# Kernel tuning notes

Hardware: AMD Instinct MI355X
Metric: run time of the kernel (lower is better)

Reference implementation:

```python
import jax, jax.numpy as jnp
import numpy as np

N_TOKENS = 2048
D_IN = 1024
D_HID = 4096
D_OUT = 1024
N_EXPERTS = 8
TOP_K = 2


def setup_inputs() -> dict:
    key = jax.random.key(0)
    ks = jax.random.split(key, 8)
    s_in = 1.0 / np.sqrt(D_IN)
    s_hid = 1.0 / np.sqrt(D_HID)
    return {
        "x": jax.random.normal(ks[0], (N_TOKENS, D_IN), dtype=jnp.float32),
        # Router Linear(D_IN, E)
        "Wr": jax.random.uniform(ks[1], (D_IN, N_EXPERTS), jnp.float32, -s_in, s_in),
        "br": jax.random.uniform(ks[2], (N_EXPERTS,), jnp.float32, -s_in, s_in),
        # Stacked expert MLP weights [E, ...]
        "W1": jax.random.uniform(ks[3], (N_EXPERTS, D_IN, D_HID), jnp.float32, -s_in, s_in),
        "b1": jax.random.uniform(ks[4], (N_EXPERTS, D_HID), jnp.float32, -s_in, s_in),
        "W2": jax.random.uniform(ks[5], (N_EXPERTS, D_HID, D_OUT), jnp.float32, -s_hid, s_hid),
        "b2": jax.random.uniform(ks[6], (N_EXPERTS, D_OUT), jnp.float32, -s_hid, s_hid),
    }


def reference(x, Wr, br, W1, b1, W2, b2):
    # Router: softmax over expert logits, then top-k
    routing = jax.nn.softmax(x @ Wr + br, axis=-1)            # [N, E]
    topk_w, topk_idx = jax.lax.top_k(routing, TOP_K)          # [N, k] each
    # Combine weights per expert: c[n, e] = sum_i topk_w[n, i] * (topk_idx[n, i] == e)
    onehot = jax.nn.one_hot(topk_idx, N_EXPERTS, dtype=x.dtype)  # [N, k, E]
    combine = jnp.einsum('nk,nke->ne', topk_w, onehot)           # [N, E]
    # Run all experts on all tokens (dense equivalent of the dispatch loop);
    # non-selected experts get combine weight 0, so math matches exactly.
    h = jax.nn.relu(jnp.einsum('nd,edh->neh', x, W1) + b1)       # [N, E, H]
    y = jnp.einsum('neh,ehd->ned', h, W2) + b2                   # [N, E, Dout]
    out = jnp.einsum('ne,ned->nd', combine, y)                   # [N, Dout]
    return out
```

## Files before the change

kernel.cpp:

```cpp
#include <hip/hip_runtime.h>
#include <hip/hip_bf16.h>

#define N_TOKENS 2048
#define D_IN 1024
#define D_HID 4096
#define D_OUT 1024
#define NE 8

typedef __attribute__((ext_vector_type(8))) short s16x8;
typedef __attribute__((ext_vector_type(4))) float f32x4;

__device__ inline unsigned short f2bf(float f) {
  union { float f; unsigned u; } v; v.f = f;
  unsigned u = v.u;
  unsigned r = u + 0x7fff + ((u >> 16) & 1);
  return (unsigned short)(r >> 16);
}

#define GLDS16(gp, lp)                                                          \
  __builtin_amdgcn_global_load_lds(                                             \
      (const __attribute__((address_space(1))) unsigned int*)(gp),              \
      (__attribute__((address_space(3))) unsigned int*)(lp), 16, 0, 0)

__global__ __launch_bounds__(256) void router_kernel(
    const float* __restrict__ x, const float* __restrict__ Wr,
    const float* __restrict__ br, int* __restrict__ cnt, int* __restrict__ tids,
    int4* __restrict__ meta, float2* __restrict__ tw) {
  int wid = threadIdx.x >> 6, lane = threadIdx.x & 63;
  int n = blockIdx.x * 4 + wid;
  const float* xr = x + (size_t)n * D_IN;
  float acc[NE];
#pragma unroll
  for (int e = 0; e < NE; e++) acc[e] = 0.f;
  for (int i = lane; i < D_IN; i += 64) {
    float xv = xr[i];
    const float4* wr = (const float4*)(Wr + (size_t)i * NE);
    float4 w0 = wr[0], w1 = wr[1];
    acc[0] += xv * w0.x; acc[1] += xv * w0.y;
    acc[2] += xv * w0.z; acc[3] += xv * w0.w;
    acc[4] += xv * w1.x; acc[5] += xv * w1.y;
    acc[6] += xv * w1.z; acc[7] += xv * w1.w;
  }
#pragma unroll
  for (int e = 0; e < NE; e++) {
#pragma unroll
    for (int s = 32; s; s >>= 1) acc[e] += __shfl_xor(acc[e], s, 64);
  }
  if (lane == 0) {
    float lg[NE], p[NE];
    float m = -1e30f;
#pragma unroll
    for (int e = 0; e < NE; e++) { lg[e] = acc[e] + br[e]; m = fmaxf(m, lg[e]); }
    float s = 0.f;
#pragma unroll
    for (int e = 0; e < NE; e++) { p[e] = expf(lg[e] - m); s += p[e]; }
    float inv = 1.f / s;
    int i0 = 0;
#pragma unroll
    for (int e = 1; e < NE; e++) if (lg[e] > lg[i0]) i0 = e;
    int i1 = (i0 == 0) ? 1 : 0;
#pragma unroll
    for (int e = 0; e < NE; e++) if (e != i0 && lg[e] > lg[i1]) i1 = e;
    int p0 = atomicAdd(&cnt[i0], 1);
    int p1 = atomicAdd(&cnt[i1], 1);
    tids[i0 * N_TOKENS + p0] = n;
    tids[i1 * N_TOKENS + p1] = n;
    meta[n] = make_int4(i0, p0, i1, p1);
    tw[n] = make_float2(p[i0] * inv, p[i1] * inv);
  }
}

__global__ __launch_bounds__(256) void convx_kernel(const float* __restrict__ x,
                                                    short* __restrict__ xb) {
  int i = (blockIdx.x * 256 + threadIdx.x) * 4;
  float4 v = *(const float4*)(x + i);
  short4 o;
  o.x = (short)f2bf(v.x); o.y = (short)f2bf(v.y);
  o.z = (short)f2bf(v.z); o.w = (short)f2bf(v.w);
  *(short4*)(xb + i) = o;
}

__global__ __launch_bounds__(256) void transconv_kernel(
    const float* __restrict__ src, short* __restrict__ dst, int R, int C) {
  __shared__ float tile[64][65];
  size_t eoff = (size_t)blockIdx.z * R * C;
  int r0 = blockIdx.y * 64, c0 = blockIdx.x * 64;
  const float* s = src + eoff + (size_t)r0 * C + c0;
  int t = threadIdx.x;
  int lc4 = (t & 15) * 4;
  int lr16 = t >> 4;
#pragma unroll
  for (int p = 0; p < 4; p++) {
    int r = p * 16 + lr16;
    float4 v = *(const float4*)(s + (size_t)r * C + lc4);
    tile[r][lc4 + 0] = v.x; tile[r][lc4 + 1] = v.y;
    tile[r][lc4 + 2] = v.z; tile[r][lc4 + 3] = v.w;
  }
  __syncthreads();
  short* d = dst + eoff + (size_t)c0 * R + r0;
  int rr4 = (t & 15) * 4;
  int cc = t >> 4;
#pragma unroll
  for (int p = 0; p < 4; p++) {
    int c = p * 16 + cc;
    short4 o;
    o.x = (short)f2bf(tile[rr4 + 0][c]);
    o.y = (short)f2bf(tile[rr4 + 1][c]);
    o.z = (short)f2bf(tile[rr4 + 2][c]);
    o.w = (short)f2bf(tile[rr4 + 3][c]);
    *(short4*)(d + (size_t)c * R + rr4) = o;
  }
}

__global__ __launch_bounds__(256) void gemm1_kernel(
    const short* __restrict__ xb,
    const short* __restrict__ W1b,
    const float* __restrict__ b1,
    const int* __restrict__ cnt, const int* __restrict__ tids,
    short* __restrict__ H) {
  const int NT_M = N_TOKENS / 128, NT_N = D_HID / 128;
  int bid0 = blockIdx.x;
  int bid = (bid0 & 7) * ((NE * NT_M * NT_N) >> 3) + (bid0 >> 3);
  int e = bid / (NT_M * NT_N);
  int r2 = bid % (NT_M * NT_N);
  int mt = r2 % NT_M, nt = r2 / NT_M;
  int ce = cnt[e];
  if (mt * 128 >= ce) return;
  int off = 0;
  for (int i = 0; i < e; i++) off += cnt[i];

  __shared__ alignas(16) short As[2][128][32];
  __shared__ alignas(16) short Bs[2][128][32];

  int lane = threadIdx.x & 63, wid = threadIdx.x >> 6;
  int wr = wid >> 1, wc = wid & 1;
  int srow = lane >> 2;
  int gch = ((lane & 3) ^ ((lane >> 3) & 3)) * 8;

  const int* tlist = tids + e * N_TOKENS + mt * 128;
  const short* a_src[2];
  const short* b_src[2];
#pragma unroll
  for (int j = 0; j < 2; j++) {
    int r = (wid + 4 * j) * 16 + srow;
    int t = (mt * 128 + r < ce) ? tlist[r] : tlist[0];
    a_src[j] = xb + (size_t)t * D_IN + gch;
    b_src[j] = W1b + (size_t)e * D_HID * D_IN + (size_t)(nt * 128 + r) * D_IN + gch;
  }

  f32x4 zero = {0.f, 0.f, 0.f, 0.f};
  f32x4 acc[4][4];
#pragma unroll
  for (int i = 0; i < 4; i++)
#pragma unroll
    for (int j = 0; j < 4; j++) acc[i][j] = zero;

#define STAGE1(ks, buf)                                                         \
  {                                                                             \
    int k0 = (ks) * 32;                                                         \
    GLDS16(a_src[0] + k0, &As[buf][wid * 16][0]);                               \
    GLDS16(a_src[1] + k0, &As[buf][(wid + 4) * 16][0]);                         \
    GLDS16(b_src[0] + k0, &Bs[buf][wid * 16][0]);                               \
    GLDS16(b_src[1] + k0, &Bs[buf][(wid + 4) * 16][0]);                         \
  }

  const int NK = D_IN / 32;
  STAGE1(0, 0);
  STAGE1(1, 1);
  int cur = 0;
  int chsh = (((lane >> 4) ^ ((lane >> 1) & 3)) & 3) * 8;
  int arow = wr * 64 + (lane & 15), brow = wc * 64 + (lane & 15);
  for (int ks = 0; ks < NK; ks++) {
    if (ks + 1 < NK) asm volatile("s_waitcnt vmcnt(4)" : : : "memory");
    else             asm volatile("s_waitcnt vmcnt(0)" : : : "memory");
    __builtin_amdgcn_s_barrier();
    s16x8 a[4], b[4];
#pragma unroll
    for (int i = 0; i < 4; i++)
      a[i] = *(const s16x8*)&As[cur][arow + i * 16][chsh];
#pragma unroll
    for (int j = 0; j < 4; j++)
      b[j] = *(const s16x8*)&Bs[cur][brow + j * 16][chsh];
#pragma unroll
    for (int i = 0; i < 4; i++)
#pragma unroll
      for (int j = 0; j < 4; j++)
        acc[i][j] = __builtin_amdgcn_mfma_f32_16x16x32_bf16(a[i], b[j], acc[i][j], 0, 0, 0);
    __builtin_amdgcn_s_barrier();
    if (ks + 2 < NK) STAGE1(ks + 2, cur);
    cur ^= 1;
  }

  int lr = (lane >> 4) * 4, lc = lane & 15;
#pragma unroll
  for (int j = 0; j < 4; j++) {
    int col = nt * 128 + wc * 64 + j * 16 + lc;
    float bias = b1[e * D_HID + col];
#pragma unroll
    for (int i = 0; i < 4; i++) {
#pragma unroll
      for (int r = 0; r < 4; r++) {
        int grow = mt * 128 + wr * 64 + i * 16 + lr + r;
        if (grow < ce) {
          float v = fmaxf(acc[i][j][r] + bias, 0.f);
          H[(size_t)(off + grow) * D_HID + col] = (short)f2bf(v);
        }
      }
    }
  }
}

__global__ __launch_bounds__(256) void gemm2_kernel(
    const short* __restrict__ H,
    const short* __restrict__ W2b,
    const int* __restrict__ cnt,
    float* __restrict__ Y) {
  const int NT_M = N_TOKENS / 128, NT_N = D_OUT / 128;
  const int PER_E = 2 * NT_M * NT_N;
  int bid0 = blockIdx.x;
  int bid = (bid0 & 7) * ((NE * PER_E) >> 3) + (bid0 >> 3);
  int e = bid / PER_E;
  int r2 = bid % PER_E;
  int kh = r2 / (NT_M * NT_N);
  int r3 = r2 % (NT_M * NT_N);
  int mt = r3 % NT_M, nt = r3 / NT_M;
  int ce = cnt[e];
  if (mt * 128 >= ce) return;
  int off = 0;
  for (int i = 0; i < e; i++) off += cnt[i];

  __shared__ alignas(16) short As[2][128][32];
  __shared__ alignas(16) short Bs[2][128][32];

  int lane = threadIdx.x & 63, wid = threadIdx.x >> 6;
  int wr = wid >> 1, wc = wid & 1;
  int srow = lane >> 2;
  int gch = ((lane & 3) ^ ((lane >> 3) & 3)) * 8;
  size_t kbase = (size_t)kh * 2048;

  const short* a_src[2];
  const short* b_src[2];
#pragma unroll
  for (int j = 0; j < 2; j++) {
    int r = (wid + 4 * j) * 16 + srow;
    int grow = mt * 128 + r;
    if (grow > ce - 1) grow = ce - 1;
    a_src[j] = H + (size_t)(off + grow) * D_HID + kbase + gch;
    b_src[j] = W2b + (size_t)e * D_OUT * D_HID + (size_t)(nt * 128 + r) * D_HID + kbase + gch;
  }

  f32x4 zero = {0.f, 0.f, 0.f, 0.f};
  f32x4 acc[4][4];
#pragma unroll
  for (int i = 0; i < 4; i++)
#pragma unroll
    for (int j = 0; j < 4; j++) acc[i][j] = zero;

#define STAGE2(ks, buf)                                                         \
  {                                                                             \
    int k0 = (ks) * 32;                                                         \
    GLDS16(a_src[0] + k0, &As[buf][wid * 16][0]);                               \
    GLDS16(a_src[1] + k0, &As[buf][(wid + 4) * 16][0]);                         \
    GLDS16(b_src[0] + k0, &Bs[buf][wid * 16][0]);                               \
    GLDS16(b_src[1] + k0, &Bs[buf][(wid + 4) * 16][0]);                         \
  }

  const int NK = 2048 / 32;
  STAGE2(0, 0);
  STAGE2(1, 1);
  int cur = 0;
  int chsh = (((lane >> 4) ^ ((lane >> 1) & 3)) & 3) * 8;
  int arow = wr * 64 + (lane & 15), brow = wc * 64 + (lane & 15);
  for (int ks = 0; ks < NK; ks++) {
    if (ks + 1 < NK) asm volatile("s_waitcnt vmcnt(4)" : : : "memory");
    else             asm volatile("s_waitcnt vmcnt(0)" : : : "memory");
    __builtin_amdgcn_s_barrier();
    s16x8 a[4], b[4];
#pragma unroll
    for (int i = 0; i < 4; i++)
      a[i] = *(const s16x8*)&As[cur][arow + i * 16][chsh];
#pragma unroll
    for (int j = 0; j < 4; j++)
      b[j] = *(const s16x8*)&Bs[cur][brow + j * 16][chsh];
#pragma unroll
    for (int i = 0; i < 4; i++)
#pragma unroll
      for (int j = 0; j < 4; j++)
        acc[i][j] = __builtin_amdgcn_mfma_f32_16x16x32_bf16(a[i], b[j], acc[i][j], 0, 0, 0);
    __builtin_amdgcn_s_barrier();
    if (ks + 2 < NK) STAGE2(ks + 2, cur);
    cur ^= 1;
  }

  float* Yh = Y + (size_t)kh * (2 * N_TOKENS) * D_OUT;
  int lr = (lane >> 4) * 4, lc = lane & 15;
#pragma unroll
  for (int j = 0; j < 4; j++) {
    int col = nt * 128 + wc * 64 + j * 16 + lc;
#pragma unroll
    for (int i = 0; i < 4; i++) {
#pragma unroll
      for (int r = 0; r < 4; r++) {
        int grow = mt * 128 + wr * 64 + i * 16 + lr + r;
        if (grow < ce) Yh[(size_t)(off + grow) * D_OUT + col] = acc[i][j][r];
      }
    }
  }
}

__global__ __launch_bounds__(256) void combine_kernel(
    const float* __restrict__ Y, const float* __restrict__ b2,
    const int* __restrict__ cnt, const int4* __restrict__ meta,
    const float2* __restrict__ tw, float* __restrict__ out) {
  const size_t YH = (size_t)(2 * N_TOKENS) * D_OUT;
  int n = blockIdx.x;
  int4 m = meta[n];
  float2 w = tw[n];
  int off0 = 0, off1 = 0;
#pragma unroll
  for (int i = 0; i < NE; i++) {
    int c = cnt[i];
    if (i < m.x) off0 += c;
    if (i < m.z) off1 += c;
  }
  size_t r0 = (size_t)(off0 + m.y) * D_OUT;
  size_t r1 = (size_t)(off1 + m.w) * D_OUT;
  const float4* y0a = (const float4*)(Y + r0);
  const float4* y0b = (const float4*)(Y + YH + r0);
  const float4* y1a = (const float4*)(Y + r1);
  const float4* y1b = (const float4*)(Y + YH + r1);
  const float4* g0 = (const float4*)(b2 + (size_t)m.x * D_OUT);
  const float4* g1 = (const float4*)(b2 + (size_t)m.z * D_OUT);
  float4* o = (float4*)(out + (size_t)n * D_OUT);
  int d = threadIdx.x;
  float4 a0 = y0a[d], a1 = y0b[d], b0 = y1a[d], b1v = y1b[d];
  float4 ba = g0[d], bb = g1[d];
  float4 r;
  r.x = w.x * (a0.x + a1.x + ba.x) + w.y * (b0.x + b1v.x + bb.x);
  r.y = w.x * (a0.y + a1.y + ba.y) + w.y * (b0.y + b1v.y + bb.y);
  r.z = w.x * (a0.z + a1.z + ba.z) + w.y * (b0.z + b1v.z + bb.z);
  r.w = w.x * (a0.w + a1.w + ba.w) + w.y * (b0.w + b1v.w + bb.w);
  o[d] = r;
}

extern "C" void kernel_launch(void* const* d_in, const int* in_sizes, int n_in,
                              void* d_out, int out_size, void* d_ws, size_t ws_size,
                              hipStream_t stream) {
  const float* x  = (const float*)d_in[0];
  const float* Wr = (const float*)d_in[1];
  const float* br = (const float*)d_in[2];
  const float* W1 = (const float*)d_in[3];
  const float* b1 = (const float*)d_in[4];
  const float* W2 = (const float*)d_in[5];
  const float* b2 = (const float*)d_in[6];
  float* out = (float*)d_out;

  char* ws = (char*)d_ws;
  size_t o = 0;
  auto alloc = [&](size_t bytes) -> void* {
    o = (o + 255) & ~(size_t)255;
    void* p = ws + o;
    o += bytes;
    return p;
  };
  int*    cnt  = (int*)alloc(NE * 4);
  int*    tids = (int*)alloc((size_t)NE * N_TOKENS * 4);
  int4*   meta = (int4*)alloc((size_t)N_TOKENS * 16);
  float2* tw   = (float2*)alloc((size_t)N_TOKENS * 8);
  short*  xb   = (short*)alloc((size_t)N_TOKENS * D_IN * 2);
  short*  W1b  = (short*)alloc((size_t)NE * D_HID * D_IN * 2);
  short*  W2b  = (short*)alloc((size_t)NE * D_OUT * D_HID * 2);
  short*  H    = (short*)alloc((size_t)2 * N_TOKENS * D_HID * 2);
  float*  Y    = (float*)alloc((size_t)2 * 2 * N_TOKENS * D_OUT * 4);
  if (o > ws_size) return;

  hipMemsetAsync(cnt, 0, NE * 4, stream);
  router_kernel<<<N_TOKENS / 4, 256, 0, stream>>>(x, Wr, br, cnt, tids, meta, tw);
  convx_kernel<<<(N_TOKENS * D_IN / 4) / 256, 256, 0, stream>>>(x, xb);
  transconv_kernel<<<dim3(D_HID / 64, D_IN / 64, NE), 256, 0, stream>>>(W1, W1b, D_IN, D_HID);
  transconv_kernel<<<dim3(D_OUT / 64, D_HID / 64, NE), 256, 0, stream>>>(W2, W2b, D_HID, D_OUT);
  gemm1_kernel<<<NE * (N_TOKENS / 128) * (D_HID / 128), 256, 0, stream>>>(xb, W1b, b1, cnt, tids, H);
  gemm2_kernel<<<NE * (N_TOKENS / 128) * (D_OUT / 128) * 2, 256, 0, stream>>>(H, W2b, cnt, Y);
  combine_kernel<<<N_TOKENS, 256, 0, stream>>>(Y, b2, cnt, meta, tw, out);
}
```

Before: 564.2 us.

## Deepen GEMM LDS pipeline to 4 stages and split gemm2 K four ways

Both expert GEMMs move from a double-buffered to a 4-deep LDS prefetch ring, with matching vmcnt waits, and raise wave priority around the MFMA block. This is meant to hide global-load latency better. gemm2's split-K goes from 2 to 4 slices, so it launches more blocks with shorter K loops and combine sums four partials. The transposed W1 buffer now shares memory with Y, which is safe only because gemm1 finishes before gemm2 writes Y. In exchange there is more LDS per block (64KB, so lower occupancy), more partial-sum traffic to write and read back, and a larger Y buffer.

```diff
diff --git a/kernel.cpp b/kernel.cpp
--- a/kernel.cpp
+++ b/kernel.cpp
@@ -129,8 +129,8 @@
   int off = 0;
   for (int i = 0; i < e; i++) off += cnt[i];
 
-  __shared__ alignas(16) short As[2][128][32];
-  __shared__ alignas(16) short Bs[2][128][32];
+  __shared__ alignas(16) short As[4][128][32];
+  __shared__ alignas(16) short Bs[4][128][32];
 
   int lane = threadIdx.x & 63, wid = threadIdx.x >> 6;
   int wr = wid >> 1, wc = wid & 1;
@@ -165,30 +165,32 @@
   }
 
   const int NK = D_IN / 32;
-  STAGE1(0, 0);
-  STAGE1(1, 1);
-  int cur = 0;
+  STAGE1(0, 0); STAGE1(1, 1); STAGE1(2, 2); STAGE1(3, 3);
   int chsh = (((lane >> 4) ^ ((lane >> 1) & 3)) & 3) * 8;
   int arow = wr * 64 + (lane & 15), brow = wc * 64 + (lane & 15);
   for (int ks = 0; ks < NK; ks++) {
-    if (ks + 1 < NK) asm volatile("s_waitcnt vmcnt(4)" : : : "memory");
-    else             asm volatile("s_waitcnt vmcnt(0)" : : : "memory");
+    if (ks < NK - 3)      asm volatile("s_waitcnt vmcnt(12)" : : : "memory");
+    else if (ks == NK - 3) asm volatile("s_waitcnt vmcnt(8)" : : : "memory");
+    else if (ks == NK - 2) asm volatile("s_waitcnt vmcnt(4)" : : : "memory");
+    else                   asm volatile("s_waitcnt vmcnt(0)" : : : "memory");
     __builtin_amdgcn_s_barrier();
+    int cb = ks & 3;
     s16x8 a[4], b[4];
 #pragma unroll
     for (int i = 0; i < 4; i++)
-      a[i] = *(const s16x8*)&As[cur][arow + i * 16][chsh];
+      a[i] = *(const s16x8*)&As[cb][arow + i * 16][chsh];
 #pragma unroll
     for (int j = 0; j < 4; j++)
-      b[j] = *(const s16x8*)&Bs[cur][brow + j * 16][chsh];
+      b[j] = *(const s16x8*)&Bs[cb][brow + j * 16][chsh];
+    __builtin_amdgcn_s_setprio(1);
 #pragma unroll
     for (int i = 0; i < 4; i++)
 #pragma unroll
       for (int j = 0; j < 4; j++)
         acc[i][j] = __builtin_amdgcn_mfma_f32_16x16x32_bf16(a[i], b[j], acc[i][j], 0, 0, 0);
+    __builtin_amdgcn_s_setprio(0);
     __builtin_amdgcn_s_barrier();
-    if (ks + 2 < NK) STAGE1(ks + 2, cur);
-    cur ^= 1;
+    if (ks + 4 < NK) STAGE1(ks + 4, cb);
   }
 
   int lr = (lane >> 4) * 4, lc = lane & 15;
@@ -216,7 +218,7 @@
     const int* __restrict__ cnt,
     float* __restrict__ Y) {
   const int NT_M = N_TOKENS / 128, NT_N = D_OUT / 128;
-  const int PER_E = 2 * NT_M * NT_N;
+  const int PER_E = 4 * NT_M * NT_N;
   int bid0 = blockIdx.x;
   int bid = (bid0 & 7) * ((NE * PER_E) >> 3) + (bid0 >> 3);
   int e = bid / PER_E;
@@ -229,14 +231,14 @@
   int off = 0;
   for (int i = 0; i < e; i++) off += cnt[i];
 
-  __shared__ alignas(16) short As[2][128][32];
-  __shared__ alignas(16) short Bs[2][128][32];
+  __shared__ alignas(16) short As[4][128][32];
+  __shared__ alignas(16) short Bs[4][128][32];
 
   int lane = threadIdx.x & 63, wid = threadIdx.x >> 6;
   int wr = wid >> 1, wc = wid & 1;
   int srow = lane >> 2;
   int gch = ((lane & 3) ^ ((lane >> 3) & 3)) * 8;
-  size_t kbase = (size_t)kh * 2048;
+  size_t kbase = (size_t)kh * 1024;
 
   const short* a_src[2];
   const short* b_src[2];
@@ -265,31 +267,33 @@
     GLDS16(b_src[1] + k0, &Bs[buf][(wid + 4) * 16][0]);                         \
   }
 
-  const int NK = 2048 / 32;
-  STAGE2(0, 0);
-  STAGE2(1, 1);
-  int cur = 0;
+  const int NK = 1024 / 32;
+  STAGE2(0, 0); STAGE2(1, 1); STAGE2(2, 2); STAGE2(3, 3);
   int chsh = (((lane >> 4) ^ ((lane >> 1) & 3)) & 3) * 8;
   int arow = wr * 64 + (lane & 15), brow = wc * 64 + (lane & 15);
   for (int ks = 0; ks < NK; ks++) {
-    if (ks + 1 < NK) asm volatile("s_waitcnt vmcnt(4)" : : : "memory");
-    else             asm volatile("s_waitcnt vmcnt(0)" : : : "memory");
+    if (ks < NK - 3)      asm volatile("s_waitcnt vmcnt(12)" : : : "memory");
+    else if (ks == NK - 3) asm volatile("s_waitcnt vmcnt(8)" : : : "memory");
+    else if (ks == NK - 2) asm volatile("s_waitcnt vmcnt(4)" : : : "memory");
+    else                   asm volatile("s_waitcnt vmcnt(0)" : : : "memory");
     __builtin_amdgcn_s_barrier();
+    int cb = ks & 3;
     s16x8 a[4], b[4];
 #pragma unroll
     for (int i = 0; i < 4; i++)
-      a[i] = *(const s16x8*)&As[cur][arow + i * 16][chsh];
+      a[i] = *(const s16x8*)&As[cb][arow + i * 16][chsh];
 #pragma unroll
     for (int j = 0; j < 4; j++)
-      b[j] = *(const s16x8*)&Bs[cur][brow + j * 16][chsh];
+      b[j] = *(const s16x8*)&Bs[cb][brow + j * 16][chsh];
+    __builtin_amdgcn_s_setprio(1);
 #pragma unroll
     for (int i = 0; i < 4; i++)
 #pragma unroll
       for (int j = 0; j < 4; j++)
         acc[i][j] = __builtin_amdgcn_mfma_f32_16x16x32_bf16(a[i], b[j], acc[i][j], 0, 0, 0);
+    __builtin_amdgcn_s_setprio(0);
     __builtin_amdgcn_s_barrier();
-    if (ks + 2 < NK) STAGE2(ks + 2, cur);
-    cur ^= 1;
+    if (ks + 4 < NK) STAGE2(ks + 4, cb);
   }
 
   float* Yh = Y + (size_t)kh * (2 * N_TOKENS) * D_OUT;
@@ -325,21 +329,23 @@
   }
   size_t r0 = (size_t)(off0 + m.y) * D_OUT;
   size_t r1 = (size_t)(off1 + m.w) * D_OUT;
-  const float4* y0a = (const float4*)(Y + r0);
-  const float4* y0b = (const float4*)(Y + YH + r0);
-  const float4* y1a = (const float4*)(Y + r1);
-  const float4* y1b = (const float4*)(Y + YH + r1);
   const float4* g0 = (const float4*)(b2 + (size_t)m.x * D_OUT);
   const float4* g1 = (const float4*)(b2 + (size_t)m.z * D_OUT);
   float4* o = (float4*)(out + (size_t)n * D_OUT);
   int d = threadIdx.x;
-  float4 a0 = y0a[d], a1 = y0b[d], b0 = y1a[d], b1v = y1b[d];
-  float4 ba = g0[d], bb = g1[d];
+  float4 s0 = g0[d], s1 = g1[d];
+#pragma unroll
+  for (int h = 0; h < 4; h++) {
+    float4 a = ((const float4*)(Y + h * YH + r0))[d];
+    float4 b = ((const float4*)(Y + h * YH + r1))[d];
+    s0.x += a.x; s0.y += a.y; s0.z += a.z; s0.w += a.w;
+    s1.x += b.x; s1.y += b.y; s1.z += b.z; s1.w += b.w;
+  }
   float4 r;
-  r.x = w.x * (a0.x + a1.x + ba.x) + w.y * (b0.x + b1v.x + bb.x);
-  r.y = w.x * (a0.y + a1.y + ba.y) + w.y * (b0.y + b1v.y + bb.y);
-  r.z = w.x * (a0.z + a1.z + ba.z) + w.y * (b0.z + b1v.z + bb.z);
-  r.w = w.x * (a0.w + a1.w + ba.w) + w.y * (b0.w + b1v.w + bb.w);
+  r.x = w.x * s0.x + w.y * s1.x;
+  r.y = w.x * s0.y + w.y * s1.y;
+  r.z = w.x * s0.z + w.y * s1.z;
+  r.w = w.x * s0.w + w.y * s1.w;
   o[d] = r;
 }
 
@@ -368,10 +374,11 @@
   int4*   meta = (int4*)alloc((size_t)N_TOKENS * 16);
   float2* tw   = (float2*)alloc((size_t)N_TOKENS * 8);
   short*  xb   = (short*)alloc((size_t)N_TOKENS * D_IN * 2);
-  short*  W1b  = (short*)alloc((size_t)NE * D_HID * D_IN * 2);
   short*  W2b  = (short*)alloc((size_t)NE * D_OUT * D_HID * 2);
   short*  H    = (short*)alloc((size_t)2 * N_TOKENS * D_HID * 2);
-  float*  Y    = (float*)alloc((size_t)2 * 2 * N_TOKENS * D_OUT * 4);
+  void*   uni  = alloc((size_t)4 * 2 * N_TOKENS * D_OUT * 4);
+  short*  W1b  = (short*)uni;
+  float*  Y    = (float*)uni;
   if (o > ws_size) return;
 
   hipMemsetAsync(cnt, 0, NE * 4, stream);
@@ -380,6 +387,6 @@
   transconv_kernel<<<dim3(D_HID / 64, D_IN / 64, NE), 256, 0, stream>>>(W1, W1b, D_IN, D_HID);
   transconv_kernel<<<dim3(D_OUT / 64, D_HID / 64, NE), 256, 0, stream>>>(W2, W2b, D_HID, D_OUT);
   gemm1_kernel<<<NE * (N_TOKENS / 128) * (D_HID / 128), 256, 0, stream>>>(xb, W1b, b1, cnt, tids, H);
-  gemm2_kernel<<<NE * (N_TOKENS / 128) * (D_OUT / 128) * 2, 256, 0, stream>>>(H, W2b, cnt, Y);
+  gemm2_kernel<<<NE * (N_TOKENS / 128) * (D_OUT / 128) * 4, 256, 0, stream>>>(H, W2b, cnt, Y);
   combine_kernel<<<N_TOKENS, 256, 0, stream>>>(Y, b2, cnt, meta, tw, out);
 }
```

Result: slower. 621.5 us (+10.2%).
